# Optimization experiments

Measured on AMD Instinct MI355X. Metric: run time of the kernel, lower is better.

The kernel has to match this reference:

```python
import jax, jax.numpy as jnp
import numpy as np

EPS = 1e-5


def setup_inputs() -> dict:
    key = jax.random.key(0)
    k1, k2, k3 = jax.random.split(key, 3)
    B, C, H, W = 64, 512, 28, 28
    G = 8
    x = jax.random.normal(k1, (B, C, H, W), dtype=jnp.float32)
    weight = jax.random.normal(k2, (G,), dtype=jnp.float32)
    bias = jax.random.normal(k3, (G,), dtype=jnp.float32)
    return {"x": x, "weight": weight, "bias": bias, "groups": G}


def reference(x, weight, bias, groups):
    B, C, H, W = x.shape
    G = groups
    cpg = C // G
    hw = H * W
    xg = x.reshape(B, G, cpg, hw)                       # [B,G,cpg,HW]
    # per-channel spatial mean
    means = jnp.mean(xg, axis=-1, keepdims=True)        # [B,G,cpg,1]
    # similarity map: dot product of each spatial vector with channel-mean vector
    s = jnp.sum(xg * means, axis=2)                     # [B,G,HW]
    # normalize s over spatial dim (population variance, eps=1e-5)
    mu = jnp.mean(s, axis=-1, keepdims=True)
    var = jnp.mean(jnp.square(s - mu), axis=-1, keepdims=True)
    t = (s - mu) * jax.lax.rsqrt(var + EPS)             # [B,G,HW]
    gate = jax.nn.sigmoid(t * weight[None, :, None] + bias[None, :, None])
    out = xg * gate[:, :, None, :]                      # broadcast gate over channels
    return out.reshape(B, C, H, W)
```

## Files before the change

kernel.cpp:

```cpp
#include <hip/hip_runtime.h>


#define HW    784
#define HW4   196
#define NG    8
#define K4    49

__global__ __launch_bounds__(256, 2)
void sge_kernel(const float* __restrict__ x,
                const float* __restrict__ weight,
                const float* __restrict__ bias,
                float* __restrict__ out) {
    __shared__ float sbuf[16 * HW];
    __shared__ float redbuf[8];

    const int t    = threadIdx.x;
    const int lane = t & 63;
    const int wave = t >> 6;
    const int j    = t & 3;

    const int bg = blockIdx.x;
    const int g  = bg & (NG - 1);
    const size_t base4 = (size_t)bg * (64 * HW4) + (size_t)(t >> 2) * HW4;

    const float4* xp = (const float4*)x + base4;
    float4 v[K4];
#pragma unroll
    for (int k = 0; k < K4; ++k) v[k] = xp[j + 4 * k];
#pragma unroll
    for (int k = 0; k < K4; ++k)
        asm volatile("" : "+v"(v[k].x), "+v"(v[k].y), "+v"(v[k].z), "+v"(v[k].w));

    float cs = 0.f;
#pragma unroll
    for (int k = 0; k < K4; ++k) cs += (v[k].x + v[k].y) + (v[k].z + v[k].w);
    cs += __shfl_xor(cs, 1, 64);
    cs += __shfl_xor(cs, 2, 64);
    const float mean_c = cs * (1.0f / (float)HW);

    const int  row    = (wave << 2) + (lane >> 4);
    float4*    srow   = (float4*)(sbuf + row * HW);
    const bool writer = ((lane >> 2) & 3) == 0;
#pragma unroll
    for (int k = 0; k < K4; ++k) {
        float4 w;
        w.x = v[k].x * mean_c; w.y = v[k].y * mean_c;
        w.z = v[k].z * mean_c; w.w = v[k].w * mean_c;
        w.x += __shfl_xor(w.x, 4, 64);  w.x += __shfl_xor(w.x, 8, 64);
        w.y += __shfl_xor(w.y, 4, 64);  w.y += __shfl_xor(w.y, 8, 64);
        w.z += __shfl_xor(w.z, 4, 64);  w.z += __shfl_xor(w.z, 8, 64);
        w.w += __shfl_xor(w.w, 4, 64);  w.w += __shfl_xor(w.w, 8, 64);
        if (writer) srow[j + 4 * k] = w;
    }
    __syncthreads();

    float s0 = 0.f, s1 = 0.f, s2 = 0.f, s3 = 0.f;
#pragma unroll
    for (int r = 0; r < 16; ++r) {
        const float* rw = sbuf + r * HW;
        s0 += rw[t];
        s1 += rw[t + 256];
        s2 += rw[t + 512];
        if (t < 16) s3 += rw[t + 768];
    }

    float rs  = s0 + s1 + s2 + s3;
    float rs2 = s0 * s0 + s1 * s1 + s2 * s2 + s3 * s3;
#pragma unroll
    for (int m = 1; m < 64; m <<= 1) {
        rs  += __shfl_xor(rs,  m, 64);
        rs2 += __shfl_xor(rs2, m, 64);
    }
    if (lane == 0) { redbuf[wave] = rs; redbuf[4 + wave] = rs2; }
    __syncthreads();

    const float sum_s  = redbuf[0] + redbuf[1] + redbuf[2] + redbuf[3];
    const float sum_s2 = redbuf[4] + redbuf[5] + redbuf[6] + redbuf[7];
    const float mu   = sum_s * (1.0f / (float)HW);
    const float var  = sum_s2 * (1.0f / (float)HW) - mu * mu;
    const float rstd = rsqrtf(var + 1e-5f);
    const float wg   = weight[g];
    const float bgv  = bias[g];

    {
        const float z0 = (s0 - mu) * rstd * wg + bgv;
        const float z1 = (s1 - mu) * rstd * wg + bgv;
        const float z2 = (s2 - mu) * rstd * wg + bgv;
        sbuf[t]       = 1.0f / (1.0f + __expf(-z0));
        sbuf[t + 256] = 1.0f / (1.0f + __expf(-z1));
        sbuf[t + 512] = 1.0f / (1.0f + __expf(-z2));
        if (t < 16) {
            const float z3 = (s3 - mu) * rstd * wg + bgv;
            sbuf[t + 768] = 1.0f / (1.0f + __expf(-z3));
        }
    }
    __syncthreads();

    const float4* gate4 = (const float4*)sbuf;
    float4* op = (float4*)out + base4;
#pragma unroll
    for (int k = 0; k < K4; ++k) {
        const float4 gv = gate4[j + 4 * k];
        float4 o;
        o.x = v[k].x * gv.x; o.y = v[k].y * gv.y;
        o.z = v[k].z * gv.z; o.w = v[k].w * gv.w;
        op[j + 4 * k] = o;
    }
}

extern "C" void kernel_launch(void* const* d_in, const int* in_sizes, int n_in,
                              void* d_out, int out_size, void* d_ws, size_t ws_size,
                              hipStream_t stream) {
    const float* x      = (const float*)d_in[0];
    const float* weight = (const float*)d_in[1];
    const float* bias   = (const float*)d_in[2];
    float* out = (float*)d_out;
    sge_kernel<<<dim3(512), dim3(256), 0, stream>>>(x, weight, bias, out);
}
```

Before: 190.4 us.

## Replace register-resident tile with multi-pass global rereads at 512 threads

The kernel no longer keeps the whole 64-channel tile in registers or builds a 16-row shared-memory partial-sum buffer. It now runs three passes over global memory: channel means, then the similarity map per spatial position (reading x weighted by shared means), then the gated output. Blocks grow to 512 threads, and register and shared-memory use drop sharply, which should raise occupancy and memory-level parallelism. The cost is reading x three times instead of once, which relies on L2 or the last-level cache to absorb the repeat reads.

```diff
diff --git a/kernel.cpp b/kernel.cpp
--- a/kernel.cpp
+++ b/kernel.cpp
@@ -3,79 +3,70 @@
 
 #define HW    784
 #define HW4   196
+#define CPG   64
 #define NG    8
-#define K4    49
 
-__global__ __launch_bounds__(256, 2)
+__global__ __launch_bounds__(512, 4)
 void sge_kernel(const float* __restrict__ x,
                 const float* __restrict__ weight,
                 const float* __restrict__ bias,
                 float* __restrict__ out) {
-    __shared__ float sbuf[16 * HW];
-    __shared__ float redbuf[8];
+    __shared__ float means[CPG];
+    __shared__ float gate[HW];
+    __shared__ float red[16];
 
     const int t    = threadIdx.x;
     const int lane = t & 63;
     const int wave = t >> 6;
-    const int j    = t & 3;
+    const int c    = t >> 3;
+    const int jj   = t & 7;
 
     const int bg = blockIdx.x;
     const int g  = bg & (NG - 1);
-    const size_t base4 = (size_t)bg * (64 * HW4) + (size_t)(t >> 2) * HW4;
-
-    const float4* xp = (const float4*)x + base4;
-    float4 v[K4];
-#pragma unroll
-    for (int k = 0; k < K4; ++k) v[k] = xp[j + 4 * k];
-#pragma unroll
-    for (int k = 0; k < K4; ++k)
-        asm volatile("" : "+v"(v[k].x), "+v"(v[k].y), "+v"(v[k].z), "+v"(v[k].w));
+    const size_t tile4 = (size_t)bg * (CPG * HW4);
+    const float4* xp = (const float4*)x + tile4 + (size_t)c * HW4;
 
     float cs = 0.f;
 #pragma unroll
-    for (int k = 0; k < K4; ++k) cs += (v[k].x + v[k].y) + (v[k].z + v[k].w);
+    for (int k = 0; k < 24; ++k) {
+        const float4 v = xp[jj + 8 * k];
+        cs += (v.x + v.y) + (v.z + v.w);
+    }
+    if (jj < 4) {
+        const float4 v = xp[192 + jj];
+        cs += (v.x + v.y) + (v.z + v.w);
+    }
     cs += __shfl_xor(cs, 1, 64);
     cs += __shfl_xor(cs, 2, 64);
-    const float mean_c = cs * (1.0f / (float)HW);
-
-    const int  row    = (wave << 2) + (lane >> 4);
-    float4*    srow   = (float4*)(sbuf + row * HW);
-    const bool writer = ((lane >> 2) & 3) == 0;
-#pragma unroll
-    for (int k = 0; k < K4; ++k) {
-        float4 w;
-        w.x = v[k].x * mean_c; w.y = v[k].y * mean_c;
-        w.z = v[k].z * mean_c; w.w = v[k].w * mean_c;
-        w.x += __shfl_xor(w.x, 4, 64);  w.x += __shfl_xor(w.x, 8, 64);
-        w.y += __shfl_xor(w.y, 4, 64);  w.y += __shfl_xor(w.y, 8, 64);
-        w.z += __shfl_xor(w.z, 4, 64);  w.z += __shfl_xor(w.z, 8, 64);
-        w.w += __shfl_xor(w.w, 4, 64);  w.w += __shfl_xor(w.w, 8, 64);
-        if (writer) srow[j + 4 * k] = w;
-    }
+    cs += __shfl_xor(cs, 4, 64);
+    if (jj == 0) means[c] = cs * (1.0f / (float)HW);
     __syncthreads();
 
-    float s0 = 0.f, s1 = 0.f, s2 = 0.f, s3 = 0.f;
-#pragma unroll
-    for (int r = 0; r < 16; ++r) {
-        const float* rw = sbuf + r * HW;
-        s0 += rw[t];
-        s1 += rw[t + 256];
-        s2 += rw[t + 512];
-        if (t < 16) s3 += rw[t + 768];
+    const float* xs = x + (size_t)bg * (CPG * HW);
+    const bool  has1 = (t + 512) < HW;
+    const int   p1   = has1 ? (t + 512) : t;
+    float s0 = 0.f, s1 = 0.f;
+#pragma unroll 8
+    for (int cc = 0; cc < CPG; ++cc) {
+        const float  mc   = means[cc];
+        const float* rowp = xs + (size_t)cc * HW;
+        s0 += rowp[t]  * mc;
+        s1 += rowp[p1] * mc;
     }
 
-    float rs  = s0 + s1 + s2 + s3;
-    float rs2 = s0 * s0 + s1 * s1 + s2 * s2 + s3 * s3;
+    float rs  = s0 + (has1 ? s1 : 0.f);
+    float rs2 = s0 * s0 + (has1 ? s1 * s1 : 0.f);
 #pragma unroll
     for (int m = 1; m < 64; m <<= 1) {
         rs  += __shfl_xor(rs,  m, 64);
         rs2 += __shfl_xor(rs2, m, 64);
     }
-    if (lane == 0) { redbuf[wave] = rs; redbuf[4 + wave] = rs2; }
+    if (lane == 0) { red[wave] = rs; red[8 + wave] = rs2; }
     __syncthreads();
 
-    const float sum_s  = redbuf[0] + redbuf[1] + redbuf[2] + redbuf[3];
-    const float sum_s2 = redbuf[4] + redbuf[5] + redbuf[6] + redbuf[7];
+    float sum_s = 0.f, sum_s2 = 0.f;
+#pragma unroll
+    for (int w = 0; w < 8; ++w) { sum_s += red[w]; sum_s2 += red[8 + w]; }
     const float mu   = sum_s * (1.0f / (float)HW);
     const float var  = sum_s2 * (1.0f / (float)HW) - mu * mu;
     const float rstd = rsqrtf(var + 1e-5f);
@@ -84,27 +75,32 @@
 
     {
         const float z0 = (s0 - mu) * rstd * wg + bgv;
-        const float z1 = (s1 - mu) * rstd * wg + bgv;
-        const float z2 = (s2 - mu) * rstd * wg + bgv;
-        sbuf[t]       = 1.0f / (1.0f + __expf(-z0));
-        sbuf[t + 256] = 1.0f / (1.0f + __expf(-z1));
-        sbuf[t + 512] = 1.0f / (1.0f + __expf(-z2));
-        if (t < 16) {
-            const float z3 = (s3 - mu) * rstd * wg + bgv;
-            sbuf[t + 768] = 1.0f / (1.0f + __expf(-z3));
+        gate[t] = 1.0f / (1.0f + __expf(-z0));
+        if (has1) {
+            const float z1 = (s1 - mu) * rstd * wg + bgv;
+            gate[t + 512] = 1.0f / (1.0f + __expf(-z1));
         }
     }
     __syncthreads();
 
-    const float4* gate4 = (const float4*)sbuf;
-    float4* op = (float4*)out + base4;
+    const float4* g4 = (const float4*)gate;
+    float4* op = (float4*)out + tile4 + (size_t)c * HW4;
 #pragma unroll
-    for (int k = 0; k < K4; ++k) {
-        const float4 gv = gate4[j + 4 * k];
+    for (int k = 0; k < 24; ++k) {
+        const float4 v  = xp[jj + 8 * k];
+        const float4 gv = g4[jj + 8 * k];
         float4 o;
-        o.x = v[k].x * gv.x; o.y = v[k].y * gv.y;
-        o.z = v[k].z * gv.z; o.w = v[k].w * gv.w;
-        op[j + 4 * k] = o;
+        o.x = v.x * gv.x; o.y = v.y * gv.y;
+        o.z = v.z * gv.z; o.w = v.w * gv.w;
+        op[jj + 8 * k] = o;
+    }
+    if (jj < 4) {
+        const float4 v  = xp[192 + jj];
+        const float4 gv = g4[192 + jj];
+        float4 o;
+        o.x = v.x * gv.x; o.y = v.y * gv.y;
+        o.z = v.z * gv.z; o.w = v.w * gv.w;
+        op[192 + jj] = o;
     }
 }
 
@@ -115,5 +111,5 @@
     const float* weight = (const float*)d_in[1];
     const float* bias   = (const float*)d_in[2];
     float* out = (float*)d_out;
-    sge_kernel<<<dim3(512), dim3(256), 0, stream>>>(x, weight, bias, out);
+    sge_kernel<<<dim3(512), dim3(512), 0, stream>>>(x, weight, bias, out);
 }
```

Result: slower. 207.0 us (+8.7%).
